# Optimization experiments

Hardware: AMD Instinct MI355X
Metric: run time of the kernel (lower is better)

## Reference

```python
import jax, jax.numpy as jnp
import numpy as np

EPS = 1e-8

def l2norm(x, axis=-1):
    norm = jnp.sqrt(jnp.sum(x * x, axis=axis, keepdims=True)) + EPS
    return x / norm

def setup_inputs() -> dict:
    key = jax.random.key(0)
    ks = jax.random.split(key, 4)
    B, Lq, Ls, d, sim_dim = 128, 128, 256, 1024, 256
    query = jax.random.normal(ks[0], (B, Lq, d), dtype=jnp.float32)
    context = jax.random.normal(ks[1], (B, Ls, d), dtype=jnp.float32)
    matrix = jax.random.uniform(ks[2], (B, Lq, d), dtype=jnp.float32)
    W = jax.random.normal(ks[3], (sim_dim, d), dtype=jnp.float32) * (1.0 / np.sqrt(d))
    b = jnp.zeros((sim_dim,), dtype=jnp.float32)
    smooth = 9
    return {"query": query, "context": context, "matrix": matrix, "W": W, "b": b, "smooth": smooth}

def reference(query, context, matrix, W, b, smooth):
    # cross_attention
    q = query * matrix                                   # (B, Lq, d)
    attn = jnp.einsum('bsd,bqd->bsq', context, q)        # (B, Ls, Lq)
    attn = jnp.where(attn >= 0, attn, 0.1 * attn)        # LeakyReLU(0.1)
    attn = l2norm(attn, axis=-1)                         # normalize over Lq
    attn = jnp.swapaxes(attn, 1, 2)                      # (B, Lq, Ls)
    attn = jax.nn.softmax(attn * smooth, axis=2)         # softmax over source
    wcontext = jnp.einsum('bqs,bsd->bqd', attn, context) # (B, Lq, d)
    wcontext = l2norm(wcontext, axis=-1)
    # alignment vector
    sim_rep = (query - wcontext) ** 2                    # (B, Lq, d)
    sim_rep = jnp.einsum('bqd,kd->bqk', sim_rep, W) + b  # Linear d -> sim_dim
    sim_rep = l2norm(sim_rep, axis=-1)
    return sim_rep
```

## Files before the change

kernel.cpp:

```cpp
#include <hip/hip_runtime.h>
#include <hip/hip_bf16.h>

constexpr int B  = 128;
constexpr int LQ = 128;
constexpr int LS = 256;
constexpr int D  = 1024;
constexpr int SD = 256;
constexpr float EPS = 1e-8f;

typedef __attribute__((ext_vector_type(8))) __bf16 bf16x8;
typedef __attribute__((ext_vector_type(4))) float f32x4;

__device__ inline ushort f2bf(float f) {
    union { float f; uint u; } v{f};
    uint r = v.u + 0x7fffu + ((v.u >> 16) & 1u);
    return (ushort)(r >> 16);
}
__device__ inline float bf2f(ushort u) {
    union { uint u; float f; } v{(uint)u << 16};
    return v.f;
}
__device__ inline uint4 pack8(float4 a, float4 b) {
    union { ushort us[8]; uint4 u4; } r;
    r.us[0]=f2bf(a.x); r.us[1]=f2bf(a.y); r.us[2]=f2bf(a.z); r.us[3]=f2bf(a.w);
    r.us[4]=f2bf(b.x); r.us[5]=f2bf(b.y); r.us[6]=f2bf(b.z); r.us[7]=f2bf(b.w);
    return r.u4;
}
__device__ inline int swz(int row, int kbyte) {
    return row * 128 + (kbyte ^ ((row & 7) << 4));
}
__device__ inline bf16x8 lds_frag(const ushort* base, int row, int kk, int lane) {
    int kbyte = kk * 64 + (lane >> 4) * 16;
    return *(const bf16x8*)((const char*)base + swz(row, kbyte));
}
__device__ inline int swz512(int row, int kbyte) {
    return row * 512 + (kbyte ^ ((row & 7) << 4));
}
__device__ inline f32x4 mfma16(bf16x8 a, bf16x8 b, f32x4 c) {
    return __builtin_amdgcn_mfma_f32_16x16x32_bf16(a, b, c, 0, 0, 0);
}

__global__ __launch_bounds__(256) void wconv_kernel(
    const float* __restrict__ W, ushort* __restrict__ Wb)
{
    size_t i = ((size_t)blockIdx.x * 256 + threadIdx.x) * 8;
    float4 a = *(const float4*)(W + i);
    float4 b = *(const float4*)(W + i + 4);
    *(uint4*)(Wb + i) = pack8(a, b);
}

__global__ __launch_bounds__(256) void qmconv_kernel(
    const float* __restrict__ query, const float* __restrict__ mat,
    ushort* __restrict__ qm)
{
    size_t i = ((size_t)blockIdx.x * 256 + threadIdx.x) * 8;
    float4 q1 = *(const float4*)(query + i), q2 = *(const float4*)(query + i + 4);
    float4 m1 = *(const float4*)(mat + i),   m2 = *(const float4*)(mat + i + 4);
    float4 p1{q1.x*m1.x, q1.y*m1.y, q1.z*m1.z, q1.w*m1.w};
    float4 p2{q2.x*m2.x, q2.y*m2.y, q2.z*m2.z, q2.w*m2.w};
    *(uint4*)(qm + i) = pack8(p1, p2);
}

__global__ __launch_bounds__(256) void cconv_kernel(
    const float* __restrict__ ctx, ushort* __restrict__ ctxB)
{
    size_t i = ((size_t)blockIdx.x * 256 + threadIdx.x) * 8;
    float4 a = *(const float4*)(ctx + i);
    float4 b = *(const float4*)(ctx + i + 4);
    *(uint4*)(ctxB + i) = pack8(a, b);
}

__global__ __launch_bounds__(512) void gemmA_kernel(
    const ushort* __restrict__ qm, const ushort* __restrict__ ctxB,
    const int* __restrict__ smooth_p, ushort* __restrict__ E)
{
    const int bid = blockIdx.x;
    const int xcd = bid & 7, idx = bid >> 3;
    const int b  = xcd * 16 + (idx >> 2);
    const int n0 = (idx & 3) * 64;
    __shared__ ushort As[2][128 * 64];
    __shared__ ushort Bs[2][64 * 64];
    __shared__ float colssP[2][64];
    __shared__ float invsm[64];
    ushort* Et = (ushort*)As;
    const int t = threadIdx.x;
    const int wv = t >> 6, l = t & 63;
    const int wq = wv >> 2, wsv = wv & 3;

    const ushort* Ab = qm   + (size_t)b * LQ * D;
    const ushort* Cb = ctxB + ((size_t)b * LS + n0) * D;
    const int r0 = t >> 3, k8 = (t & 7) * 8;

    f32x4 acc[4] = {};
    uint4 a0, a1, b0;

    a0 = *(const uint4*)(Ab + (size_t)r0 * D + k8);
    a1 = *(const uint4*)(Ab + (size_t)(r0 + 64) * D + k8);
    b0 = *(const uint4*)(Cb + (size_t)r0 * D + k8);
    *(uint4*)((char*)As[0] + swz(r0, k8 * 2))      = a0;
    *(uint4*)((char*)As[0] + swz(r0 + 64, k8 * 2)) = a1;
    *(uint4*)((char*)Bs[0] + swz(r0, k8 * 2))      = b0;
    __syncthreads();

    int cur = 0;
#pragma unroll 1
    for (int ks = 0; ks < 15; ++ks) {
        const int k0 = (ks + 1) * 64;
        a0 = *(const uint4*)(Ab + (size_t)r0 * D + k0 + k8);
        a1 = *(const uint4*)(Ab + (size_t)(r0 + 64) * D + k0 + k8);
        b0 = *(const uint4*)(Cb + (size_t)r0 * D + k0 + k8);
#pragma unroll
        for (int kk = 0; kk < 2; ++kk) {
            bf16x8 bfr = lds_frag(Bs[cur], wsv * 16 + (l & 15), kk, l);
#pragma unroll
            for (int i = 0; i < 4; ++i) {
                bf16x8 af = lds_frag(As[cur], wq * 64 + i * 16 + (l & 15), kk, l);
                acc[i] = mfma16(af, bfr, acc[i]);
            }
        }
        *(uint4*)((char*)As[cur ^ 1] + swz(r0, k8 * 2))      = a0;
        *(uint4*)((char*)As[cur ^ 1] + swz(r0 + 64, k8 * 2)) = a1;
        *(uint4*)((char*)Bs[cur ^ 1] + swz(r0, k8 * 2))      = b0;
        __syncthreads();
        cur ^= 1;
    }
#pragma unroll
    for (int kk = 0; kk < 2; ++kk) {
        bf16x8 bfr = lds_frag(Bs[cur], wsv * 16 + (l & 15), kk, l);
#pragma unroll
        for (int i = 0; i < 4; ++i) {
            bf16x8 af = lds_frag(As[cur], wq * 64 + i * 16 + (l & 15), kk, l);
            acc[i] = mfma16(af, bfr, acc[i]);
        }
    }

    float csum = 0.f;
#pragma unroll
    for (int i = 0; i < 4; ++i)
#pragma unroll
        for (int r = 0; r < 4; ++r) {
            float v = acc[i][r];
            v = v >= 0.f ? v : 0.1f * v;
            acc[i][r] = v;
            csum += v * v;
        }
    csum += __shfl_xor(csum, 16);
    csum += __shfl_xor(csum, 32);
    if (l < 16) colssP[wq][wsv * 16 + l] = csum;
    __syncthreads();
    const float sm = (float)(*smooth_p);
    if (t < 64) invsm[t] = sm / (sqrtf(colssP[0][t] + colssP[1][t]) + EPS);
    __syncthreads();
    const float invc = invsm[wsv * 16 + (l & 15)];
#pragma unroll
    for (int i = 0; i < 4; ++i)
#pragma unroll
        for (int r = 0; r < 4; ++r) {
            int row = wq * 64 + i * 16 + (l >> 4) * 4 + r;
            Et[row * 72 + wsv * 16 + (l & 15)] = f2bf(__expf(acc[i][r] * invc));
        }
    __syncthreads();
    ushort* Eg = E + (size_t)b * LQ * LS + n0;
#pragma unroll
    for (int j = 0; j < 2; ++j) {
        int c = t + j * 512;
        int row = c >> 3, s8 = (c & 7) * 8;
        *(uint4*)(Eg + (size_t)row * LS + s8) = *(const uint4*)(Et + row * 72 + s8);
    }
}

__global__ __launch_bounds__(512) void pv_kernel(
    const ushort* __restrict__ E, const ushort* __restrict__ ctxB,
    ushort* __restrict__ wctx, float* __restrict__ rowssP)
{
    const int bid = blockIdx.x;
    const int xcd = bid & 7, idx = bid >> 3;
    const int b  = xcd * 16 + (idx >> 1);
    const int dh = idx & 1;
    const int dglob0 = dh * 512;

    __shared__ ushort Es[128 * 256];
    __shared__ ushort Bs[64 * 264];
    __shared__ float rsumL[128];
    __shared__ float rinv[128];
    __shared__ float rowssL[128][4];

    const int t = threadIdx.x;
    const int wv = t >> 6, l = t & 63;
    const int wq = wv >> 2, wd = wv & 3;

    const ushort* Eb = E + (size_t)b * LQ * LS;
    const int cc = t & 31, rr = t >> 5;
    float part[8];
#pragma unroll
    for (int p = 0; p < 8; ++p) {
        int row = rr + p * 16;
        uint4 v = *(const uint4*)(Eb + (size_t)row * LS + cc * 8);
        *(uint4*)((char*)Es + swz512(row, cc * 16)) = v;
        const ushort* us = (const ushort*)&v;
        float s = 0.f;
#pragma unroll
        for (int j = 0; j < 8; ++j) s += bf2f(us[j]);
        part[p] = s;
    }
    rowssL[t >> 2][t & 3] = 0.f;
#pragma unroll
    for (int p = 0; p < 8; ++p) {
        float s = part[p];
        s += __shfl_xor(s, 1);  s += __shfl_xor(s, 2);
        s += __shfl_xor(s, 4);  s += __shfl_xor(s, 8);
        s += __shfl_xor(s, 16);
        if ((l & 31) == 0) rsumL[rr + p * 16] = s;
    }

    const ushort* Cb = ctxB + (size_t)b * LS * D + dglob0;
    const int sr = t >> 4, c4 = (t & 15) * 4;
    uint2 cr[8];
#pragma unroll
    for (int p = 0; p < 8; ++p)
        cr[p] = *(const uint2*)(Cb + (size_t)(p * 32 + sr) * D + c4);

    __syncthreads();
    if (t < 128) rinv[t] = 1.0f / rsumL[t];

#pragma unroll
    for (int p = 0; p < 8; ++p) {
        int s = p * 32 + sr;
        const ushort* us = (const ushort*)&cr[p];
        Bs[(c4 + 0) * 264 + s] = us[0];
        Bs[(c4 + 1) * 264 + s] = us[1];
        Bs[(c4 + 2) * 264 + s] = us[2];
        Bs[(c4 + 3) * 264 + s] = us[3];
    }
    __syncthreads();

    ushort* Ob = wctx + (size_t)b * LQ * D + dglob0;

#pragma unroll 1
    for (int dt = 0; dt < 8; ++dt) {
        if (dt < 7) {
#pragma unroll
            for (int p = 0; p < 8; ++p)
                cr[p] = *(const uint2*)(Cb + (size_t)(p * 32 + sr) * D + (dt + 1) * 64 + c4);
        }
        f32x4 acc[4] = {};
#pragma unroll
        for (int kk = 0; kk < 8; ++kk) {
            const ushort* bp = Bs + (wd * 16 + (l & 15)) * 264 + kk * 32 + (l >> 4) * 8;
            bf16x8 bfr = *(const bf16x8*)bp;
#pragma unroll
            for (int i = 0; i < 4; ++i) {
                bf16x8 af = *(const bf16x8*)((const char*)Es +
                    swz512(wq * 64 + i * 16 + (l & 15), kk * 64 + (l >> 4) * 16));
                acc[i] = mfma16(af, bfr, acc[i]);
            }
        }
#pragma unroll
        for (int i = 0; i < 4; ++i)
#pragma unroll
            for (int r = 0; r < 4; ++r) {
                int row = wq * 64 + i * 16 + (l >> 4) * 4 + r;
                float wval = acc[i][r] * rinv[row];
                float p2 = wval * wval;
                p2 += __shfl_xor(p2, 1); p2 += __shfl_xor(p2, 2);
                p2 += __shfl_xor(p2, 4); p2 += __shfl_xor(p2, 8);
                if ((l & 15) == 0) rowssL[row][wd] += p2;
                Ob[(size_t)row * D + dt * 64 + wd * 16 + (l & 15)] = f2bf(wval);
            }
        __syncthreads();
        if (dt < 7) {
#pragma unroll
            for (int p = 0; p < 8; ++p) {
                int s = p * 32 + sr;
                const ushort* us = (const ushort*)&cr[p];
                Bs[(c4 + 0) * 264 + s] = us[0];
                Bs[(c4 + 1) * 264 + s] = us[1];
                Bs[(c4 + 2) * 264 + s] = us[2];
                Bs[(c4 + 3) * 264 + s] = us[3];
            }
            __syncthreads();
        }
    }
    if (t < 128)
        rowssP[(size_t)b * 256 + dh * 128 + t] =
            rowssL[t][0] + rowssL[t][1] + rowssL[t][2] + rowssL[t][3];
}

__global__ __launch_bounds__(512) void gemm3_kernel(
    const ushort* __restrict__ wctx, const float* __restrict__ query,
    const float* __restrict__ rowssP, const ushort* __restrict__ Wb,
    const float* __restrict__ bias, float* __restrict__ out)
{
    const int m0 = blockIdx.x * 64;
    const int b  = blockIdx.y;
    __shared__ ushort As[64 * 64];
    __shared__ ushort Bs[256 * 64];
    __shared__ float red[64][4];
    __shared__ float invr[64];
    const int t = threadIdx.x;
    const int w = t >> 6, l = t & 63;
    const int wm = (w >> 2) * 32, wn = (w & 3) * 64;

    const int arow = t >> 3, ako = (t & 7) * 8;
    const float r0v = rowssP[(size_t)b * 256 + m0 + arow];
    const float r1v = rowssP[(size_t)b * 256 + 128 + m0 + arow];
    const float ivq = 1.0f / (sqrtf(r0v + r1v) + EPS);
    const float* Qp  = query + ((size_t)b * LQ + m0 + arow) * D + ako;
    const ushort* Wp = wctx  + ((size_t)b * LQ + m0 + arow) * D + ako;

    f32x4 acc[2][4] = {};

    for (int k0 = 0; k0 < D; k0 += 64) {
        if (k0) __syncthreads();
        {
            uint4 wu = *(const uint4*)(Wp + k0);
            float4 q1 = *(const float4*)(Qp + k0);
            float4 q2 = *(const float4*)(Qp + k0 + 4);
            float d0 = q1.x - bf2f((ushort)(wu.x & 0xffff)) * ivq;
            float d1 = q1.y - bf2f((ushort)(wu.x >> 16))    * ivq;
            float d2 = q1.z - bf2f((ushort)(wu.y & 0xffff)) * ivq;
            float d3 = q1.w - bf2f((ushort)(wu.y >> 16))    * ivq;
            float d4 = q2.x - bf2f((ushort)(wu.z & 0xffff)) * ivq;
            float d5 = q2.y - bf2f((ushort)(wu.z >> 16))    * ivq;
            float d6 = q2.z - bf2f((ushort)(wu.w & 0xffff)) * ivq;
            float d7 = q2.w - bf2f((ushort)(wu.w >> 16))    * ivq;
            float4 s1{d0*d0, d1*d1, d2*d2, d3*d3};
            float4 s2{d4*d4, d5*d5, d6*d6, d7*d7};
            *(uint4*)((char*)As + swz(arow, ako * 2)) = pack8(s1, s2);
        }
#pragma unroll
        for (int j = 0; j < 4; ++j) {
            int c = t + j * 512;
            int row = c >> 3, ko = (c & 7) * 8;
            *(uint4*)((char*)Bs + swz(row, ko * 2)) =
                *(const uint4*)(Wb + (size_t)row * D + k0 + ko);
        }
        __syncthreads();
#pragma unroll
        for (int kk = 0; kk < 2; ++kk) {
            bf16x8 af[2], bfr[4];
#pragma unroll
            for (int i = 0; i < 2; ++i) af[i] = lds_frag(As, wm + i * 16 + (l & 15), kk, l);
#pragma unroll
            for (int n = 0; n < 4; ++n) bfr[n] = lds_frag(Bs, wn + n * 16 + (l & 15), kk, l);
#pragma unroll
            for (int i = 0; i < 2; ++i)
#pragma unroll
                for (int n = 0; n < 4; ++n) acc[i][n] = mfma16(af[i], bfr[n], acc[i][n]);
        }
    }
#pragma unroll
    for (int n = 0; n < 4; ++n) {
        float bv = bias[wn + n * 16 + (l & 15)];
#pragma unroll
        for (int i = 0; i < 2; ++i)
#pragma unroll
            for (int r = 0; r < 4; ++r) acc[i][n][r] += bv;
    }
#pragma unroll
    for (int i = 0; i < 2; ++i)
#pragma unroll
        for (int r = 0; r < 4; ++r) {
            float p = 0.f;
#pragma unroll
            for (int n = 0; n < 4; ++n) p += acc[i][n][r] * acc[i][n][r];
#pragma unroll
            for (int off = 1; off < 16; off <<= 1) p += __shfl_xor(p, off);
            int rowl = wm + i * 16 + (l >> 4) * 4 + r;
            if ((l & 15) == 0) red[rowl][w & 3] = p;
        }
    __syncthreads();
    if (t < 64) {
        float s = red[t][0] + red[t][1] + red[t][2] + red[t][3];
        invr[t] = 1.0f / (sqrtf(s) + EPS);
    }
    __syncthreads();
    float* Ob = out + ((size_t)b * LQ + m0) * SD;
#pragma unroll
    for (int i = 0; i < 2; ++i)
#pragma unroll
        for (int r = 0; r < 4; ++r) {
            int rowl = wm + i * 16 + (l >> 4) * 4 + r;
            float iv = invr[rowl];
#pragma unroll
            for (int n = 0; n < 4; ++n) {
                int col = wn + n * 16 + (l & 15);
                Ob[(size_t)rowl * SD + col] = acc[i][n][r] * iv;
            }
        }
}

extern "C" void kernel_launch(void* const* d_in, const int* in_sizes, int n_in,
                              void* d_out, int out_size, void* d_ws, size_t ws_size,
                              hipStream_t stream)
{
    const float* query  = (const float*)d_in[0];
    const float* ctx    = (const float*)d_in[1];
    const float* mat    = (const float*)d_in[2];
    const float* W      = (const float*)d_in[3];
    const float* bias   = (const float*)d_in[4];
    const int*   smooth = (const int*)d_in[5];
    float* out = (float*)d_out;

    char* ws = (char*)d_ws;
    ushort* ctxB   = (ushort*)ws;
    ushort* qm     = (ushort*)(ws + (size_t)64 * 1024 * 1024);
    ushort* wctx   = qm;
    ushort* E      = (ushort*)(ws + (size_t)96 * 1024 * 1024);
    ushort* Wb     = (ushort*)(ws + (size_t)104 * 1024 * 1024);
    float*  rowssP = (float*)(ws + (size_t)(104 * 1024 + 512) * 1024);

    wconv_kernel<<<dim3(SD * D / (256 * 8)), 256, 0, stream>>>(W, Wb);
    qmconv_kernel<<<dim3((size_t)B * LQ * D / (256 * 8)), 256, 0, stream>>>(query, mat, qm);
    cconv_kernel<<<dim3((size_t)B * LS * D / (256 * 8)), 256, 0, stream>>>(ctx, ctxB);
    gemmA_kernel<<<dim3(512), 512, 0, stream>>>(qm, ctxB, smooth, E);
    pv_kernel<<<dim3(256), 512, 0, stream>>>(E, ctxB, wctx, rowssP);
    gemm3_kernel<<<dim3(2, B), 512, 0, stream>>>(wctx, query, rowssP, Wb, bias, out);
}
```

Before: 177.6 us.

## Fuse context fp32-to-bf16 conversion into first GEMM and write E directly

Removes the separate context conversion kernel. The first GEMM now loads fp32 context, packs it to bf16 for its shared-memory tile, and writes the bf16 copy to the workspace for the later PV kernel. This saves a full read and write of the bf16 context plus one launch. The LDS-staged coalesced store of E is replaced with direct scattered 2-byte global stores, and launch bounds with min 2 blocks per CU are added to the PV and final GEMM kernels, which may cause register pressure or spills.

```diff
diff --git a/kernel.cpp b/kernel.cpp
--- a/kernel.cpp
+++ b/kernel.cpp
@@ -61,18 +61,10 @@
     *(uint4*)(qm + i) = pack8(p1, p2);
 }
 
-__global__ __launch_bounds__(256) void cconv_kernel(
-    const float* __restrict__ ctx, ushort* __restrict__ ctxB)
-{
-    size_t i = ((size_t)blockIdx.x * 256 + threadIdx.x) * 8;
-    float4 a = *(const float4*)(ctx + i);
-    float4 b = *(const float4*)(ctx + i + 4);
-    *(uint4*)(ctxB + i) = pack8(a, b);
-}
-
 __global__ __launch_bounds__(512) void gemmA_kernel(
-    const ushort* __restrict__ qm, const ushort* __restrict__ ctxB,
-    const int* __restrict__ smooth_p, ushort* __restrict__ E)
+    const ushort* __restrict__ qm, const float* __restrict__ ctx,
+    const int* __restrict__ smooth_p, ushort* __restrict__ E,
+    ushort* __restrict__ ctxB)
 {
     const int bid = blockIdx.x;
     const int xcd = bid & 7, idx = bid >> 3;
@@ -82,24 +74,30 @@
     __shared__ ushort Bs[2][64 * 64];
     __shared__ float colssP[2][64];
     __shared__ float invsm[64];
-    ushort* Et = (ushort*)As;
     const int t = threadIdx.x;
     const int wv = t >> 6, l = t & 63;
     const int wq = wv >> 2, wsv = wv & 3;
 
-    const ushort* Ab = qm   + (size_t)b * LQ * D;
-    const ushort* Cb = ctxB + ((size_t)b * LS + n0) * D;
+    const ushort* Ab = qm  + (size_t)b * LQ * D;
+    const float*  Cb = ctx + ((size_t)b * LS + n0) * D;
+    ushort*      CBb = ctxB + ((size_t)b * LS + n0) * D;
     const int r0 = t >> 3, k8 = (t & 7) * 8;
 
     f32x4 acc[4] = {};
-    uint4 a0, a1, b0;
+    uint4 a0, a1;
+    float4 c0, c1;
 
     a0 = *(const uint4*)(Ab + (size_t)r0 * D + k8);
     a1 = *(const uint4*)(Ab + (size_t)(r0 + 64) * D + k8);
-    b0 = *(const uint4*)(Cb + (size_t)r0 * D + k8);
-    *(uint4*)((char*)As[0] + swz(r0, k8 * 2))      = a0;
-    *(uint4*)((char*)As[0] + swz(r0 + 64, k8 * 2)) = a1;
-    *(uint4*)((char*)Bs[0] + swz(r0, k8 * 2))      = b0;
+    c0 = *(const float4*)(Cb + (size_t)r0 * D + k8);
+    c1 = *(const float4*)(Cb + (size_t)r0 * D + k8 + 4);
+    {
+        uint4 pc = pack8(c0, c1);
+        *(uint4*)((char*)As[0] + swz(r0, k8 * 2))      = a0;
+        *(uint4*)((char*)As[0] + swz(r0 + 64, k8 * 2)) = a1;
+        *(uint4*)((char*)Bs[0] + swz(r0, k8 * 2))      = pc;
+        *(uint4*)(CBb + (size_t)r0 * D + k8) = pc;
+    }
     __syncthreads();
 
     int cur = 0;
@@ -108,7 +106,8 @@
         const int k0 = (ks + 1) * 64;
         a0 = *(const uint4*)(Ab + (size_t)r0 * D + k0 + k8);
         a1 = *(const uint4*)(Ab + (size_t)(r0 + 64) * D + k0 + k8);
-        b0 = *(const uint4*)(Cb + (size_t)r0 * D + k0 + k8);
+        c0 = *(const float4*)(Cb + (size_t)r0 * D + k0 + k8);
+        c1 = *(const float4*)(Cb + (size_t)r0 * D + k0 + k8 + 4);
 #pragma unroll
         for (int kk = 0; kk < 2; ++kk) {
             bf16x8 bfr = lds_frag(Bs[cur], wsv * 16 + (l & 15), kk, l);
@@ -118,9 +117,13 @@
                 acc[i] = mfma16(af, bfr, acc[i]);
             }
         }
-        *(uint4*)((char*)As[cur ^ 1] + swz(r0, k8 * 2))      = a0;
-        *(uint4*)((char*)As[cur ^ 1] + swz(r0 + 64, k8 * 2)) = a1;
-        *(uint4*)((char*)Bs[cur ^ 1] + swz(r0, k8 * 2))      = b0;
+        {
+            uint4 pc = pack8(c0, c1);
+            *(uint4*)((char*)As[cur ^ 1] + swz(r0, k8 * 2))      = a0;
+            *(uint4*)((char*)As[cur ^ 1] + swz(r0 + 64, k8 * 2)) = a1;
+            *(uint4*)((char*)Bs[cur ^ 1] + swz(r0, k8 * 2))      = pc;
+            *(uint4*)(CBb + (size_t)r0 * D + k0 + k8) = pc;
+        }
         __syncthreads();
         cur ^= 1;
     }
@@ -152,24 +155,17 @@
     if (t < 64) invsm[t] = sm / (sqrtf(colssP[0][t] + colssP[1][t]) + EPS);
     __syncthreads();
     const float invc = invsm[wsv * 16 + (l & 15)];
+    ushort* Eb = E + (size_t)b * LQ * LS + n0 + wsv * 16 + (l & 15);
 #pragma unroll
     for (int i = 0; i < 4; ++i)
 #pragma unroll
         for (int r = 0; r < 4; ++r) {
             int row = wq * 64 + i * 16 + (l >> 4) * 4 + r;
-            Et[row * 72 + wsv * 16 + (l & 15)] = f2bf(__expf(acc[i][r] * invc));
-        }
-    __syncthreads();
-    ushort* Eg = E + (size_t)b * LQ * LS + n0;
-#pragma unroll
-    for (int j = 0; j < 2; ++j) {
-        int c = t + j * 512;
-        int row = c >> 3, s8 = (c & 7) * 8;
-        *(uint4*)(Eg + (size_t)row * LS + s8) = *(const uint4*)(Et + row * 72 + s8);
-    }
-}
-
-__global__ __launch_bounds__(512) void pv_kernel(
+            Eb[(size_t)row * LS] = f2bf(__expf(acc[i][r] * invc));
+        }
+}
+
+__global__ __launch_bounds__(512, 2) void pv_kernel(
     const ushort* __restrict__ E, const ushort* __restrict__ ctxB,
     ushort* __restrict__ wctx, float* __restrict__ rowssP)
 {
@@ -286,7 +282,7 @@
             rowssL[t][0] + rowssL[t][1] + rowssL[t][2] + rowssL[t][3];
 }
 
-__global__ __launch_bounds__(512) void gemm3_kernel(
+__global__ __launch_bounds__(512, 2) void gemm3_kernel(
     const ushort* __restrict__ wctx, const float* __restrict__ query,
     const float* __restrict__ rowssP, const ushort* __restrict__ Wb,
     const float* __restrict__ bias, float* __restrict__ out)
@@ -412,8 +408,7 @@
 
     wconv_kernel<<<dim3(SD * D / (256 * 8)), 256, 0, stream>>>(W, Wb);
     qmconv_kernel<<<dim3((size_t)B * LQ * D / (256 * 8)), 256, 0, stream>>>(query, mat, qm);
-    cconv_kernel<<<dim3((size_t)B * LS * D / (256 * 8)), 256, 0, stream>>>(ctx, ctxB);
-    gemmA_kernel<<<dim3(512), 512, 0, stream>>>(qm, ctxB, smooth, E);
+    gemmA_kernel<<<dim3(512), 512, 0, stream>>>(qm, ctx, smooth, E, ctxB);
     pv_kernel<<<dim3(256), 512, 0, stream>>>(E, ctxB, wctx, rowssP);
     gemm3_kernel<<<dim3(2, B), 512, 0, stream>>>(wctx, query, rowssP, Wb, bias, out);
 }
```

After: 170.4 us. 1.04x faster.
